# Optimization experiments

Hardware: AMD Instinct MI355X
Metric: run time of the kernel (lower is better)

The kernel has to match this reference:

```python
import jax, jax.numpy as jnp
import numpy as np

N_NODES = 131072
N_EDGES = 1048576
N_FEAT = 8
H = 128
H6 = 256
N_PROB = 64


def _gru_cell(m, h, Wih, Whh, bih, bhh):
    # PyTorch GRUCell semantics
    gi = m @ Wih.T + bih  # [N, 3H]
    gh = h @ Whh.T + bhh
    i_r, i_z, i_n = jnp.split(gi, 3, axis=-1)
    h_r, h_z, h_n = jnp.split(gh, 3, axis=-1)
    r = jax.nn.sigmoid(i_r + h_r)
    z = jax.nn.sigmoid(i_z + h_z)
    n = jnp.tanh(i_n + r * h_n)
    return (1.0 - z) * n + z * h


def _gated_graph_conv(x, src, dst, ew, W, Wih, Whh, bih, bhh):
    # PyG GatedGraphConv(out_channels=H, num_layers=2); in_channels == out_channels so no padding
    h = x
    for l in range(2):
        t = h @ W[l]                      # node-level transform [N, H]
        msg = t[src] * ew[:, None]        # gather + edge scaling [E, H]
        agg = jax.ops.segment_sum(msg, dst, num_segments=x.shape[0])  # scatter-add
        h = _gru_cell(agg, h, Wih, Whh, bih, bhh)
    return h


def _forward(G, edge_index, edge_weight, edge_attribute, segment_ids,
             W_emb1, b_emb1, W_emb2, b_emb2,
             conv1_W, conv1_Wih, conv1_Whh, conv1_bih, conv1_bhh,
             conv2_W, conv2_Wih, conv2_Whh, conv2_bih, conv2_bhh,
             W_g1, b_g1, W_g2, b_g2, W_l, b_l, W_l2, b_l2, W_l3, b_l3):
    src, dst = edge_index[0], edge_index[1]
    x = jax.nn.relu(G @ W_emb1 + b_emb1)
    x = jax.nn.relu(x @ W_emb2 + b_emb2)
    x = jax.nn.relu(_gated_graph_conv(x, src, dst, edge_weight, conv1_W, conv1_Wih, conv1_Whh, conv1_bih, conv1_bhh))
    x = jax.nn.relu(_gated_graph_conv(x, src, dst, edge_weight, conv2_W, conv2_Wih, conv2_Whh, conv2_bih, conv2_bhh))
    x = jax.nn.relu(x @ W_g1 + b_g1)
    x = x @ W_g2 + b_g2                   # node embeddings [N, H]
    # per-problem segment mean (replaces the python loop over contiguous slices)
    sums = jax.ops.segment_sum(x, segment_ids, num_segments=N_PROB)
    counts = jax.ops.segment_sum(jnp.ones((x.shape[0], 1), x.dtype), segment_ids, num_segments=N_PROB)
    gmean = sums / jnp.maximum(counts, 1.0)
    u = jnp.concatenate([x, gmean[segment_ids]], axis=-1)  # [N, 2H]
    u = jax.nn.relu(u @ W_l + b_l)
    u = jax.nn.relu(u @ W_l2 + b_l2)
    u = u @ W_l3 + b_l3                   # [N, 1]
    return u


def setup_inputs() -> dict:
    key = jax.random.key(0)
    ks = jax.random.split(key, 40)
    s = 0.05
    rn = lambda k, shp: (jax.random.normal(k, shp, jnp.float32) * s)
    inp = {}
    inp["G"] = jax.random.normal(ks[0], (N_NODES, N_FEAT), jnp.float32)
    inp["edge_index"] = jax.random.randint(ks[1], (2, N_EDGES), 0, N_NODES, jnp.int32)
    inp["edge_weight"] = jax.random.uniform(ks[2], (N_EDGES,), jnp.float32)
    inp["edge_attribute"] = jax.random.normal(ks[3], (N_EDGES,), jnp.float32)
    inp["segment_ids"] = jnp.sort(jax.random.randint(ks[4], (N_NODES,), 0, N_PROB, jnp.int32))
    inp["W_emb1"] = rn(ks[5], (N_FEAT, H)); inp["b_emb1"] = jnp.zeros((H,), jnp.float32)
    inp["W_emb2"] = rn(ks[6], (H, H));      inp["b_emb2"] = jnp.zeros((H,), jnp.float32)
    inp["conv1_W"] = rn(ks[7], (2, H, H))
    inp["conv1_Wih"] = rn(ks[8], (3 * H, H)); inp["conv1_Whh"] = rn(ks[9], (3 * H, H))
    inp["conv1_bih"] = jnp.zeros((3 * H,), jnp.float32); inp["conv1_bhh"] = jnp.zeros((3 * H,), jnp.float32)
    inp["conv2_W"] = rn(ks[10], (2, H, H))
    inp["conv2_Wih"] = rn(ks[11], (3 * H, H)); inp["conv2_Whh"] = rn(ks[12], (3 * H, H))
    inp["conv2_bih"] = jnp.zeros((3 * H,), jnp.float32); inp["conv2_bhh"] = jnp.zeros((3 * H,), jnp.float32)
    inp["W_g1"] = rn(ks[13], (H, H)); inp["b_g1"] = jnp.zeros((H,), jnp.float32)
    inp["W_g2"] = rn(ks[14], (H, H)); inp["b_g2"] = jnp.zeros((H,), jnp.float32)
    inp["W_l"] = rn(ks[15], (2 * H, H6)); inp["b_l"] = jnp.zeros((H6,), jnp.float32)
    inp["W_l2"] = rn(ks[16], (H6, H)); inp["b_l2"] = jnp.zeros((H,), jnp.float32)
    inp["W_l3"] = rn(ks[17], (H, 1)); inp["b_l3"] = jnp.zeros((1,), jnp.float32)
    return inp


def reference(G, edge_index, edge_weight, edge_attribute, segment_ids,
              W_emb1, b_emb1, W_emb2, b_emb2,
              conv1_W, conv1_Wih, conv1_Whh, conv1_bih, conv1_bhh,
              conv2_W, conv2_Wih, conv2_Whh, conv2_bih, conv2_bhh,
              W_g1, b_g1, W_g2, b_g2, W_l, b_l, W_l2, b_l2, W_l3, b_l3):
    return _forward(G, edge_index, edge_weight, edge_attribute, segment_ids,
                    W_emb1, b_emb1, W_emb2, b_emb2,
                    conv1_W, conv1_Wih, conv1_Whh, conv1_bih, conv1_bhh,
                    conv2_W, conv2_Wih, conv2_Whh, conv2_bih, conv2_bhh,
                    W_g1, b_g1, W_g2, b_g2, W_l, b_l, W_l2, b_l2, W_l3, b_l3)
```

## Files before the change

### kernel.cpp

```cpp
#include <hip/hip_runtime.h>
#include <cstdint>
#include <cstddef>

#define NNODES 131072
#define NEDGES 1048576
#define NPROB  64

typedef _Float16 half8 __attribute__((ext_vector_type(8)));
typedef _Float16 half4v __attribute__((ext_vector_type(4)));
typedef _Float16 half2v __attribute__((ext_vector_type(2)));
typedef float float4v __attribute__((ext_vector_type(4)));

__device__ __forceinline__ float fsigm(float x) {
    return __builtin_amdgcn_rcpf(1.0f + __expf(-x));
}
__device__ __forceinline__ float ftanh(float x) {
    return 1.0f - 2.0f * __builtin_amdgcn_rcpf(__expf(2.0f * x) + 1.0f);
}

__device__ __forceinline__ void async16(void* lds, const void* g) {
    __builtin_amdgcn_global_load_lds(
        (const __attribute__((address_space(1))) uint32_t*)g,
        (__attribute__((address_space(3))) uint32_t*)lds, 16, 0, 0);
}

__global__ __launch_bounds__(256) void tr_cvt2(const float* __restrict__ s0,
    const float* __restrict__ s1, _Float16* __restrict__ dst)
{
    int i = blockIdx.x * 256 + threadIdx.x;
    int half = i >> 14, r = i & 16383;
    int m = r >> 7, k = r & 127;
    const float* s = half ? s1 : s0;
    dst[i] = (_Float16)s[(size_t)k * 128 + m];
}

__global__ __launch_bounds__(256) void tr_cvt(const float* __restrict__ src,
    _Float16* __restrict__ dst, int K, int M, int sstride)
{
    int i = blockIdx.x * 256 + threadIdx.x;
    if (i < M * K) {
        int m = i / K, k = i % K;
        dst[i] = (_Float16)src[(size_t)k * sstride + m];
    }
}

__global__ __launch_bounds__(256) void cvt16_2(const float* __restrict__ a,
    const float* __restrict__ b, _Float16* __restrict__ d)
{
    int i = blockIdx.x * 256 + threadIdx.x;
    d[i] = (_Float16)((i < 49152) ? a[i] : b[i - 49152]);
}

__global__ __launch_bounds__(256) void combine_gru4(const float* __restrict__ W1ih,
    const float* __restrict__ W1, const float* __restrict__ W2ih,
    const float* __restrict__ W2, _Float16* __restrict__ outw)
{
    int i = blockIdx.x * 256 + threadIdx.x;
    int set = i / 49152, r = i - set * 49152;
    int g = r >> 7, j = r & 127;
    const float* Wih = (set < 2) ? W1ih : W2ih;
    const float* W = (set == 0) ? W1 : (set == 1) ? W1 + 16384
                   : (set == 2) ? W2 : W2 + 16384;
    const float* a = Wih + (size_t)g * 128;
    const float* b = W + (size_t)j * 128;
    float s = 0.0f;
#pragma unroll 8
    for (int k = 0; k < 128; ++k) s = fmaf(a[k], b[k], s);
    outw[i] = (_Float16)s;
}

__global__ __launch_bounds__(256) void combine_headA(const float* __restrict__ Wg2,
    const float* __restrict__ Wl, _Float16* __restrict__ At)
{
    int i = blockIdx.x * 256 + threadIdx.x;
    int m = i >> 7, j = i & 127;
    float s = 0.0f;
#pragma unroll 8
    for (int k = 0; k < 128; ++k)
        s = fmaf(Wg2[(size_t)j * 128 + k], Wl[(size_t)k * 256 + m], s);
    At[i] = (_Float16)s;
}

__global__ __launch_bounds__(256) void combine_headB(const float* __restrict__ Wg2,
    const float* __restrict__ Wl, float* __restrict__ Bf)
{
    int i = blockIdx.x * 256 + threadIdx.x;
    int t = i >> 8, m = i & 255;
    float s = 0.0f;
#pragma unroll 8
    for (int k = 0; k < 128; ++k)
        s = fmaf(Wg2[(size_t)t * 128 + k], Wl[(size_t)(128 + k) * 256 + m], s);
    Bf[i] = s;
}

__global__ __launch_bounds__(256) void combine_c(const float* __restrict__ bg2,
    const float* __restrict__ Wl, const float* __restrict__ bl, float* __restrict__ cvec)
{
    int m = threadIdx.x;
    float s = bl[m];
#pragma unroll 8
    for (int k = 0; k < 128; ++k)
        s = fmaf(bg2[k], Wl[(size_t)k * 256 + m] + Wl[(size_t)(128 + k) * 256 + m], s);
    cvec[m] = s;
}

__global__ __launch_bounds__(256) void deg_hist(const int* __restrict__ dst,
                                                int* __restrict__ deg)
{
    int e = blockIdx.x * 256 + threadIdx.x;
    atomicAdd(&deg[dst[e]], 1);
}

__global__ __launch_bounds__(256) void scan1(const int* __restrict__ deg,
    int* __restrict__ offs, int* __restrict__ bsum)
{
    __shared__ int s[256];
    int b = blockIdx.x, tid = threadIdx.x;
    int4 v = ((const int4*)deg)[b * 256 + tid];
    int t0 = v.x, t1 = t0 + v.y, t2 = t1 + v.z, t3 = t2 + v.w;
    s[tid] = t3;
    __syncthreads();
    for (int off = 1; off < 256; off <<= 1) {
        int x = (tid >= off) ? s[tid - off] : 0;
        __syncthreads();
        if (tid >= off) s[tid] += x;
        __syncthreads();
    }
    int excl = tid ? s[tid - 1] : 0;
    int4 o; o.x = excl; o.y = excl + t0; o.z = excl + t1; o.w = excl + t2;
    ((int4*)offs)[b * 256 + tid] = o;
    if (tid == 255) bsum[b] = s[255];
}

__global__ __launch_bounds__(128) void scan2(int* __restrict__ bsum)
{
    __shared__ int s[128];
    int tid = threadIdx.x;
    s[tid] = bsum[tid];
    __syncthreads();
    for (int off = 1; off < 128; off <<= 1) {
        int x = (tid >= off) ? s[tid - off] : 0;
        __syncthreads();
        if (tid >= off) s[tid] += x;
        __syncthreads();
    }
    bsum[tid] = tid ? s[tid - 1] : 0;
}

__global__ __launch_bounds__(256) void scan3(int* __restrict__ offs,
    const int* __restrict__ bsum, int* __restrict__ pos)
{
    int i = blockIdx.x * 256 + threadIdx.x;
    int v = offs[i] + bsum[i >> 10];
    offs[i] = v;
    pos[i] = v;
    if (i == 0) offs[NNODES] = NEDGES;
}

__global__ __launch_bounds__(256) void csr_fill(const int* __restrict__ src,
    const int* __restrict__ dst, const float* __restrict__ ew,
    int* __restrict__ pos, int2* __restrict__ csr)
{
    int e = blockIdx.x * 256 + threadIdx.x;
    int slot = atomicAdd(&pos[dst[e]], 1);
    unsigned long long pk = (unsigned long long)(unsigned)src[e]
                          | ((unsigned long long)__float_as_uint(ew[e]) << 32);
    __builtin_nontemporal_store(pk, (unsigned long long*)csr + slot);
}

__global__ __launch_bounds__(256) void gather_agg(const _Float16* __restrict__ t,
    const int2* __restrict__ csr, const int* __restrict__ offs,
    _Float16* __restrict__ agg)
{
    int node = blockIdx.x * 4 + (threadIdx.x >> 6);
    int lane = threadIdx.x & 63;
    int i = offs[node], end = offs[node + 1];
    float a0 = 0.0f, a1 = 0.0f;
    for (; i + 4 <= end; i += 4) {
        int2 e0 = csr[i], e1 = csr[i + 1], e2 = csr[i + 2], e3 = csr[i + 3];
        half2v v0 = *(const half2v*)(t + (size_t)e0.x * 128 + lane * 2);
        half2v v1 = *(const half2v*)(t + (size_t)e1.x * 128 + lane * 2);
        half2v v2 = *(const half2v*)(t + (size_t)e2.x * 128 + lane * 2);
        half2v v3 = *(const half2v*)(t + (size_t)e3.x * 128 + lane * 2);
        float w0 = __int_as_float(e0.y), w1 = __int_as_float(e1.y);
        float w2 = __int_as_float(e2.y), w3 = __int_as_float(e3.y);
        a0 = fmaf((float)v0[0], w0, a0); a1 = fmaf((float)v0[1], w0, a1);
        a0 = fmaf((float)v1[0], w1, a0); a1 = fmaf((float)v1[1], w1, a1);
        a0 = fmaf((float)v2[0], w2, a0); a1 = fmaf((float)v2[1], w2, a1);
        a0 = fmaf((float)v3[0], w3, a0); a1 = fmaf((float)v3[1], w3, a1);
    }
    for (; i < end; ++i) {
        int2 e = csr[i];
        float w = __int_as_float(e.y);
        half2v v = *(const half2v*)(t + (size_t)e.x * 128 + lane * 2);
        a0 = fmaf((float)v[0], w, a0);
        a1 = fmaf((float)v[1], w, a1);
    }
    half2v o; o[0] = (_Float16)a0; o[1] = (_Float16)a1;
    *(half2v*)(agg + (size_t)node * 128 + lane * 2) = o;
}

__global__ __launch_bounds__(256) void emb1_kernel(const float* __restrict__ G,
    const float* __restrict__ W1, const float* __restrict__ b1, _Float16* __restrict__ Y)
{
    int idx = blockIdx.x * 256 + threadIdx.x;
    int n = idx >> 7, c = idx & 127;
    const float* g = G + (size_t)n * 8;
    float y = b1[c];
#pragma unroll
    for (int k = 0; k < 8; ++k) y = fmaf(g[k], W1[k * 128 + c], y);
    Y[(size_t)n * 128 + c] = (_Float16)fmaxf(y, 0.0f);
}

template<int K, int MCH, bool INF16, bool RELU, bool SEGADD, bool FINAL>
__global__ __launch_bounds__(256, 2) void gemm_mfma(
    const void* __restrict__ Xin, int xstride,
    const _Float16* __restrict__ Wt,
    const float* __restrict__ bias,
    _Float16* __restrict__ out1, int ostride,
    const float* __restrict__ gproj, const int* __restrict__ seg,
    const float* __restrict__ wl3, const float* __restrict__ bl3p,
    float* __restrict__ outf)
{
    constexpr int ROWB = 2 * K;
    constexpr int SPR  = K / 8;
    __shared__ __align__(16) char Xs[128 * ROWB];
    __shared__ __align__(16) char Ws[128 * ROWB];
    const int tid = threadIdx.x, wid = tid >> 6, l = tid & 63;
    const int lr = l & 15, lk = l >> 4;
    const int wrow = wid * 32;

    for (int mc = 0; mc < MCH; ++mc) {
        __syncthreads();
        {
            const _Float16* wsrc = Wt + (size_t)mc * 128 * K;
            for (int s0 = wid * 64; s0 < 128 * SPR; s0 += 256) {
                int s = s0 + l;
                int row = s / SPR, sub = s % SPR;
                int ksub = sub ^ (row & 7);
                async16(Ws + s0 * 16, (const char*)(wsrc + (size_t)row * K) + ksub * 16);
            }
        }
        asm volatile("s_waitcnt vmcnt(0)" ::: "memory");
        __syncthreads();

        half8 bfr[32];
        if constexpr (K == 128) {
#pragma unroll
            for (int ct = 0; ct < 8; ++ct)
#pragma unroll
                for (int ks = 0; ks < 4; ++ks) {
                    int row = ct * 16 + lr;
                    bfr[ct * 4 + ks] = *(const half8*)(Ws + row * ROWB +
                        ((ks * 64 + lk * 16) ^ ((row & 7) << 4)));
                }
        }

        for (int t = blockIdx.x; t < NNODES / 128; t += gridDim.x) {
            const int nbase = t * 128;
            __syncthreads();
            if constexpr (INF16) {
                const _Float16* xsrc = (const _Float16*)Xin;
                for (int s0 = wid * 64; s0 < 128 * SPR; s0 += 256) {
                    int s = s0 + l;
                    int row = s / SPR, sub = s % SPR;
                    int ksub = sub ^ (row & 7);
                    async16(Xs + s0 * 16,
                            (const char*)(xsrc + (size_t)(nbase + row) * xstride) + ksub * 16);
                }
                asm volatile("s_waitcnt vmcnt(0)" ::: "memory");
            } else {
                const float* xsrc = (const float*)Xin;
                for (int s = tid; s < 128 * SPR; s += 256) {
                    int row = s / SPR, sub = s % SPR;
                    int ksub = sub ^ (row & 7);
                    const float* p = xsrc + (size_t)(nbase + row) * xstride + ksub * 8;
                    float4 u = ((const float4*)p)[0];
                    float4 v = ((const float4*)p)[1];
                    half8 hv;
                    hv[0] = (_Float16)u.x; hv[1] = (_Float16)u.y;
                    hv[2] = (_Float16)u.z; hv[3] = (_Float16)u.w;
                    hv[4] = (_Float16)v.x; hv[5] = (_Float16)v.y;
                    hv[6] = (_Float16)v.z; hv[7] = (_Float16)v.w;
                    *(half8*)(Xs + s * 16) = hv;
                }
            }
            __syncthreads();

            float4v acc[2][8];
#pragma unroll
            for (int i = 0; i < 2; ++i)
#pragma unroll
                for (int j = 0; j < 8; ++j)
#pragma unroll
                    for (int q = 0; q < 4; ++q) acc[i][j][q] = 0.0f;

            if constexpr (K == 128) {
#pragma unroll
                for (int rt = 0; rt < 2; ++rt) {
                    half8 a[4];
                    int row = wrow + rt * 16 + lr;
#pragma unroll
                    for (int ks = 0; ks < 4; ++ks)
                        a[ks] = *(const half8*)(Xs + row * ROWB +
                            ((ks * 64 + lk * 16) ^ ((row & 7) << 4)));
#pragma unroll
                    for (int ct = 0; ct < 8; ++ct)
#pragma unroll
                        for (int ks = 0; ks < 4; ++ks)
                            acc[rt][ct] = __builtin_amdgcn_mfma_f32_16x16x32_f16(
                                a[ks], bfr[ct * 4 + ks], acc[rt][ct], 0, 0, 0);
                }
            } else {
#pragma unroll
                for (int kc = 0; kc < 2; ++kc) {
#pragma unroll
                    for (int ct = 0; ct < 8; ++ct)
#pragma unroll
                        for (int ks = 0; ks < 4; ++ks) {
                            int row = ct * 16 + lr;
                            bfr[ct * 4 + ks] = *(const half8*)(Ws + row * ROWB +
                                (((kc * 4 + ks) * 64 + lk * 16) ^ ((row & 7) << 4)));
                        }
#pragma unroll
                    for (int rt = 0; rt < 2; ++rt) {
                        half8 a[4];
                        int row = wrow + rt * 16 + lr;
#pragma unroll
                        for (int ks = 0; ks < 4; ++ks)
                            a[ks] = *(const half8*)(Xs + row * ROWB +
                                (((kc * 4 + ks) * 64 + lk * 16) ^ ((row & 7) << 4)));
#pragma unroll
                        for (int ct = 0; ct < 8; ++ct)
#pragma unroll
                            for (int ks = 0; ks < 4; ++ks)
                                acc[rt][ct] = __builtin_amdgcn_mfma_f32_16x16x32_f16(
                                    a[ks], bfr[ct * 4 + ks], acc[rt][ct], 0, 0, 0);
                    }
                }
            }

            if constexpr (FINAL) {
                const float bl3v = bl3p[0];
                float part[2][4];
#pragma unroll
                for (int rt = 0; rt < 2; ++rt)
#pragma unroll
                    for (int j = 0; j < 4; ++j) part[rt][j] = 0.0f;
#pragma unroll
                for (int rt = 0; rt < 2; ++rt)
#pragma unroll
                for (int ct = 0; ct < 8; ++ct) {
                    const int col = ct * 16 + lr;
                    const float wv = wl3[col];
                    const float bv = bias[col];
#pragma unroll
                    for (int j = 0; j < 4; ++j) {
                        float v = fmaxf(acc[rt][ct][j] + bv, 0.0f);
                        part[rt][j] = fmaf(v, wv, part[rt][j]);
                    }
                }
#pragma unroll
                for (int rt = 0; rt < 2; ++rt)
#pragma unroll
                for (int j = 0; j < 4; ++j) {
                    float s = part[rt][j];
                    s += __shfl_xor(s, 1);
                    s += __shfl_xor(s, 2);
                    s += __shfl_xor(s, 4);
                    s += __shfl_xor(s, 8);
                    if (lr == 0)
                        outf[nbase + wrow + rt * 16 + lk * 4 + j] = s + bl3v;
                }
            } else {
#pragma unroll
                for (int rt = 0; rt < 2; ++rt)
#pragma unroll
                for (int ct = 0; ct < 8; ++ct) {
                    const int col = ct * 16 + lr;
                    float bv = 0.0f;
                    if (bias) bv = bias[mc * 128 + col];
#pragma unroll
                    for (int j = 0; j < 4; ++j) {
                        const int n = nbase + wrow + rt * 16 + lk * 4 + j;
                        float v = acc[rt][ct][j] + bv;
                        if constexpr (SEGADD)
                            v += gproj[(size_t)seg[n] * 256 + mc * 128 + col];
                        if constexpr (RELU) v = fmaxf(v, 0.0f);
                        out1[(size_t)n * ostride + mc * 128 + col] = (_Float16)v;
                    }
                }
            }
        }
    }
}

__global__ __launch_bounds__(512, 2) void gru_fused(
    const _Float16* __restrict__ agg,
    _Float16* h,
    const _Float16* __restrict__ Wc,
    const _Float16* __restrict__ Whh,
    const float* __restrict__ bih, const float* __restrict__ bhh,
    int relu_out)
{
    __shared__ __align__(16) char As[128 * 256];
    __shared__ __align__(16) char Hs[128 * 256];
    __shared__ __align__(16) char Wb[2][128 * 256];
    const int tid = threadIdx.x, wid = tid >> 6, l = tid & 63;
    const int lr = l & 15, lk = l >> 4;
    const int wr = wid >> 1, wc = wid & 1;
    const int nbase = blockIdx.x * 128;

    auto stageT = [&](char* dst, const _Float16* src) {
        for (int s0 = wid * 64; s0 < 2048; s0 += 512) {
            int s = s0 + l;
            int row = s >> 4, sub = s & 15;
            int ksub = sub ^ (row & 7);
            async16(dst + s0 * 16, (const char*)(src + (size_t)row * 128) + ksub * 16);
        }
    };

    stageT(As, agg + (size_t)nbase * 128);
    stageT(Hs, h + (size_t)nbase * 128);
    stageT(Wb[0], Wc);

    float4v accA[2][4], accB[2][4], rg[2][4], zg[2][4];
    half8 aAg[2][4], aH[2][4];

#pragma unroll
    for (int c = 0; c < 6; ++c) {
        asm volatile("s_waitcnt vmcnt(0)" ::: "memory");
        __syncthreads();
        if (c < 5) {
            const int nc = c + 1;
            const _Float16* wsrc = ((nc & 1) ? Whh : Wc) + (size_t)(nc >> 1) * 16384;
            stageT(Wb[nc & 1], wsrc);
        }
        if (c == 0) {
#pragma unroll
            for (int rt = 0; rt < 2; ++rt) {
                const int row = wr * 32 + rt * 16 + lr;
#pragma unroll
                for (int ks = 0; ks < 4; ++ks) {
                    const int off = row * 256 + ((ks * 64 + lk * 16) ^ ((row & 7) << 4));
                    aAg[rt][ks] = *(const half8*)(As + off);
                    aH[rt][ks]  = *(const half8*)(Hs + off);
                }
            }
        }

        auto& af  = (c & 1) ? aH : aAg;
        auto& acc = (c & 1) ? accB : accA;
#pragma unroll
        for (int rt = 0; rt < 2; ++rt)
#pragma unroll
            for (int ct = 0; ct < 4; ++ct)
#pragma unroll
                for (int q = 0; q < 4; ++q) acc[rt][ct][q] = 0.0f;

        const char* wb = Wb[c & 1];
#pragma unroll
        for (int ct = 0; ct < 4; ++ct) {
            const int rowb = wc * 64 + ct * 16 + lr;
#pragma unroll
            for (int ks = 0; ks < 4; ++ks) {
                half8 b = *(const half8*)(wb + rowb * 256 +
                    ((ks * 64 + lk * 16) ^ ((rowb & 7) << 4)));
                acc[0][ct] = __builtin_amdgcn_mfma_f32_16x16x32_f16(af[0][ks], b, acc[0][ct], 0, 0, 0);
                acc[1][ct] = __builtin_amdgcn_mfma_f32_16x16x32_f16(af[1][ks], b, acc[1][ct], 0, 0, 0);
            }
        }

        if (c == 1) {
#pragma unroll
            for (int rt = 0; rt < 2; ++rt)
#pragma unroll
            for (int ct = 0; ct < 4; ++ct) {
                const int col = wc * 64 + ct * 16 + lr;
                const float bb = bih[col] + bhh[col];
#pragma unroll
                for (int j = 0; j < 4; ++j)
                    rg[rt][ct][j] = fsigm(accA[rt][ct][j] + accB[rt][ct][j] + bb);
            }
        } else if (c == 3) {
#pragma unroll
            for (int rt = 0; rt < 2; ++rt)
#pragma unroll
            for (int ct = 0; ct < 4; ++ct) {
                const int col = wc * 64 + ct * 16 + lr;
                const float bb = bih[128 + col] + bhh[128 + col];
#pragma unroll
                for (int j = 0; j < 4; ++j)
                    zg[rt][ct][j] = fsigm(accA[rt][ct][j] + accB[rt][ct][j] + bb);
            }
        } else if (c == 5) {
#pragma unroll
            for (int rt = 0; rt < 2; ++rt)
#pragma unroll
            for (int ct = 0; ct < 4; ++ct) {
                const int col = wc * 64 + ct * 16 + lr;
                const float bi = bih[256 + col], bh = bhh[256 + col];
                const int c2 = col * 2;
#pragma unroll
                for (int j = 0; j < 4; ++j) {
                    const int row = wr * 32 + rt * 16 + lk * 4 + j;
                    const int n = nbase + row;
                    float nv = ftanh(accA[rt][ct][j] + bi +
                                     rg[rt][ct][j] * (accB[rt][ct][j] + bh));
                    float hold = (float)*(const _Float16*)(Hs + row * 256 +
                        (((c2 >> 4) ^ (row & 7)) << 4) + (c2 & 15));
                    float z = zg[rt][ct][j];
                    float hn = (1.0f - z) * nv + z * hold;
                    if (relu_out) hn = fmaxf(hn, 0.0f);
                    h[(size_t)n * 128 + col] = (_Float16)hn;
                }
            }
        }
    }
}

__global__ __launch_bounds__(256) void seg_sum(const _Float16* __restrict__ x,
    const int* __restrict__ seg, float* __restrict__ sums, float* __restrict__ counts)
{
    int cg = threadIdx.x & 31, rs = threadIdx.x >> 5;
    int r0 = blockIdx.x * 256 + rs * 32;
    float a0 = 0, a1 = 0, a2 = 0, a3 = 0, cnt = 0;
    int cur = seg[r0];
    for (int i = 0; i < 32; ++i) {
        int n = r0 + i;
        int p = seg[n];
        if (p != cur) {
            atomicAdd(&sums[(size_t)cur * 128 + cg * 4 + 0], a0);
            atomicAdd(&sums[(size_t)cur * 128 + cg * 4 + 1], a1);
            atomicAdd(&sums[(size_t)cur * 128 + cg * 4 + 2], a2);
            atomicAdd(&sums[(size_t)cur * 128 + cg * 4 + 3], a3);
            if (cg == 0) atomicAdd(&counts[cur], cnt);
            a0 = a1 = a2 = a3 = 0; cnt = 0; cur = p;
        }
        half4v v = *(const half4v*)(x + (size_t)n * 128 + cg * 4);
        a0 += (float)v[0]; a1 += (float)v[1]; a2 += (float)v[2]; a3 += (float)v[3];
        cnt += 1.0f;
    }
    atomicAdd(&sums[(size_t)cur * 128 + cg * 4 + 0], a0);
    atomicAdd(&sums[(size_t)cur * 128 + cg * 4 + 1], a1);
    atomicAdd(&sums[(size_t)cur * 128 + cg * 4 + 2], a2);
    atomicAdd(&sums[(size_t)cur * 128 + cg * 4 + 3], a3);
    if (cg == 0) atomicAdd(&counts[cur], cnt);
}

__global__ __launch_bounds__(256) void gproj2_kernel(const float* __restrict__ sums,
    const float* __restrict__ counts, const float* __restrict__ Bf,
    const float* __restrict__ cvec, float* __restrict__ gproj2)
{
    __shared__ float gm[128];
    int p = blockIdx.x, m = threadIdx.x;
    if (m < 128) gm[m] = sums[(size_t)p * 128 + m] / fmaxf(counts[p], 1.0f);
    __syncthreads();
    float acc = cvec[m];
#pragma unroll 8
    for (int k = 0; k < 128; ++k)
        acc = fmaf(gm[k], Bf[(size_t)k * 256 + m], acc);
    gproj2[(size_t)p * 256 + m] = acc;
}

extern "C" void kernel_launch(void* const* d_in, const int* in_sizes, int n_in,
                              void* d_out, int out_size, void* d_ws, size_t ws_size,
                              hipStream_t stream)
{
    (void)in_sizes; (void)n_in; (void)out_size; (void)ws_size;

    const float* G     = (const float*)d_in[0];
    const int*   ei    = (const int*)d_in[1];
    const float* ew    = (const float*)d_in[2];
    const int*   seg   = (const int*)d_in[4];
    const float* Wemb1 = (const float*)d_in[5];  const float* bemb1 = (const float*)d_in[6];
    const float* Wemb2 = (const float*)d_in[7];  const float* bemb2 = (const float*)d_in[8];
    const float* c1W   = (const float*)d_in[9];
    const float* c1Wih = (const float*)d_in[10]; const float* c1Whh = (const float*)d_in[11];
    const float* c1bih = (const float*)d_in[12]; const float* c1bhh = (const float*)d_in[13];
    const float* c2W   = (const float*)d_in[14];
    const float* c2Wih = (const float*)d_in[15]; const float* c2Whh = (const float*)d_in[16];
    const float* c2bih = (const float*)d_in[17]; const float* c2bhh = (const float*)d_in[18];
    const float* Wg1   = (const float*)d_in[19]; const float* bg1   = (const float*)d_in[20];
    const float* Wg2   = (const float*)d_in[21]; const float* bg2   = (const float*)d_in[22];
    const float* Wl    = (const float*)d_in[23]; const float* bl    = (const float*)d_in[24];
    const float* Wl2   = (const float*)d_in[25]; const float* bl2   = (const float*)d_in[26];
    const float* Wl3   = (const float*)d_in[27]; const float* bl3   = (const float*)d_in[28];

    const int* srcp = ei;
    const int* dstp = ei + NEDGES;

    char* ws = (char*)d_ws;
    const size_t NBH = (size_t)NNODES * 128 * 2;
    const size_t U1B = (size_t)NNODES * 256 * 2;

    _Float16* hA   = (_Float16*)ws;
    _Float16* hB   = (_Float16*)(ws + NBH);
    _Float16* u1   = (_Float16*)(ws + 2 * NBH);
    _Float16* aggH = (_Float16*)(ws + 2 * NBH + U1B);
    char*     aux  = ws + 3 * NBH + U1B;
    float* sums    = (float*)aux;
    float* counts  = (float*)(aux + 32768);
    float* gproj2  = (float*)(aux + 33792);
    int*   deg     = (int*)(aux + 33792 + 65536);
    int*   offs    = deg + NNODES;
    int*   pos     = offs + NNODES + 64;
    int2*  csr     = (int2*)(pos + NNODES);
    char*  wtb     = (char*)csr + (size_t)NEDGES * 8;

    _Float16* wt_emb2 = (_Float16*)wtb;
    _Float16* wt_g1   = wt_emb2 + 16384;
    _Float16* wt_l2   = wt_g1 + 16384;
    _Float16* wt_hh1  = wt_l2 + 32768;
    _Float16* wt_hh2  = wt_hh1 + 49152;
    _Float16* wc0     = wt_hh2 + 49152;
    _Float16* At      = wc0 + 4 * 49152;
    float*    Bf      = (float*)(At + 32768);
    float*    cvec    = Bf + 32768;

    tr_cvt2<<<128, 256, 0, stream>>>(Wemb2, Wg1, wt_emb2);
    tr_cvt<<<128, 256, 0, stream>>>(Wl2, wt_l2, 256, 128, 128);
    cvt16_2<<<384, 256, 0, stream>>>(c1Whh, c2Whh, wt_hh1);
    combine_gru4<<<768, 256, 0, stream>>>(c1Wih, c1W, c2Wih, c2W, wc0);
    combine_headA<<<128, 256, 0, stream>>>(Wg2, Wl, At);
    combine_headB<<<128, 256, 0, stream>>>(Wg2, Wl, Bf);
    combine_c<<<1, 256, 0, stream>>>(bg2, Wl, bl, cvec);

    hipMemsetAsync(deg, 0, NNODES * 4, stream);
    deg_hist<<<NEDGES / 256, 256, 0, stream>>>(dstp, deg);
    scan1<<<128, 256, 0, stream>>>(deg, offs, pos);
    scan2<<<1, 128, 0, stream>>>(pos);
    scan3<<<NNODES / 256, 256, 0, stream>>>(offs, pos, deg);
    csr_fill<<<NEDGES / 256, 256, 0, stream>>>(srcp, dstp, ew, deg, csr);

    emb1_kernel<<<NNODES * 128 / 256, 256, 0, stream>>>(G, Wemb1, bemb1, hB);
    gemm_mfma<128, 1, true, true, false, false><<<512, 256, 0, stream>>>(
        hB, 128, wt_emb2, bemb2, hA, 128, nullptr, nullptr, nullptr, nullptr, nullptr);

    const _Float16* wcs[2][2] = { { wc0, wc0 + 49152 }, { wc0 + 2 * 49152, wc0 + 3 * 49152 } };
    const _Float16* whh[2] = { wt_hh1, wt_hh2 };
    const float* bihs[2] = { c1bih, c2bih };
    const float* bhhs[2] = { c1bhh, c2bhh };
    for (int cv = 0; cv < 2; ++cv) {
        for (int lyr = 0; lyr < 2; ++lyr) {
            gather_agg<<<NNODES / 4, 256, 0, stream>>>(hA, csr, offs, aggH);
            gru_fused<<<NNODES / 128, 512, 0, stream>>>(
                aggH, hA, wcs[cv][lyr], whh[cv], bihs[cv], bhhs[cv], (lyr == 1) ? 1 : 0);
        }
    }

    gemm_mfma<128, 1, true, true, false, false><<<512, 256, 0, stream>>>(
        hA, 128, wt_g1, bg1, hB, 128, nullptr, nullptr, nullptr, nullptr, nullptr);

    hipMemsetAsync(sums, 0, 33792, stream);
    seg_sum<<<NNODES / 256, 256, 0, stream>>>(hB, seg, sums, counts);
    gproj2_kernel<<<NPROB, 256, 0, stream>>>(sums, counts, Bf, cvec, gproj2);

    gemm_mfma<128, 2, true, true, true, false><<<512, 256, 0, stream>>>(
        hB, 128, At, nullptr, u1, 256, gproj2, seg, nullptr, nullptr, nullptr);
    gemm_mfma<256, 1, true, true, false, true><<<256, 256, 0, stream>>>(
        u1, 256, wt_l2, bl2, nullptr, 0, nullptr, nullptr, Wl3, bl3, (float*)d_out);
}
```

Before: 934.9 us.

## Shrink GRU tile to 64 rows with single weight buffer, deepen gather unroll

The fused GRU kernel now handles 64 nodes per block instead of 128 and keeps one weight buffer instead of two. This cuts shared memory per block so more blocks fit per CU (launch bounds raised to 4). The cost is that weight prefetch no longer overlaps with MFMA compute, each weight chunk is re-staged by twice as many blocks, and an extra barrier is added per chunk. Separately, the gather kernel gets an 8-way unrolled loop to keep more independent loads in flight, and the CSR fill drops its nontemporal packed store for a plain int2 store.

```diff
diff --git a/kernel.cpp b/kernel.cpp
--- a/kernel.cpp
+++ b/kernel.cpp
@@ -163,9 +163,7 @@
 {
     int e = blockIdx.x * 256 + threadIdx.x;
     int slot = atomicAdd(&pos[dst[e]], 1);
-    unsigned long long pk = (unsigned long long)(unsigned)src[e]
-                          | ((unsigned long long)__float_as_uint(ew[e]) << 32);
-    __builtin_nontemporal_store(pk, (unsigned long long*)csr + slot);
+    csr[slot] = make_int2(src[e], __float_as_int(ew[e]));
 }
 
 __global__ __launch_bounds__(256) void gather_agg(const _Float16* __restrict__ t,
@@ -176,18 +174,35 @@
     int lane = threadIdx.x & 63;
     int i = offs[node], end = offs[node + 1];
     float a0 = 0.0f, a1 = 0.0f;
+    for (; i + 8 <= end; i += 8) {
+        int2 e[8];
+#pragma unroll
+        for (int k = 0; k < 8; ++k) e[k] = csr[i + k];
+        half2v v[8];
+#pragma unroll
+        for (int k = 0; k < 8; ++k)
+            v[k] = *(const half2v*)(t + (size_t)e[k].x * 128 + lane * 2);
+#pragma unroll
+        for (int k = 0; k < 8; ++k) {
+            float w = __int_as_float(e[k].y);
+            a0 = fmaf((float)v[k][0], w, a0);
+            a1 = fmaf((float)v[k][1], w, a1);
+        }
+    }
     for (; i + 4 <= end; i += 4) {
-        int2 e0 = csr[i], e1 = csr[i + 1], e2 = csr[i + 2], e3 = csr[i + 3];
-        half2v v0 = *(const half2v*)(t + (size_t)e0.x * 128 + lane * 2);
-        half2v v1 = *(const half2v*)(t + (size_t)e1.x * 128 + lane * 2);
-        half2v v2 = *(const half2v*)(t + (size_t)e2.x * 128 + lane * 2);
-        half2v v3 = *(const half2v*)(t + (size_t)e3.x * 128 + lane * 2);
-        float w0 = __int_as_float(e0.y), w1 = __int_as_float(e1.y);
-        float w2 = __int_as_float(e2.y), w3 = __int_as_float(e3.y);
-        a0 = fmaf((float)v0[0], w0, a0); a1 = fmaf((float)v0[1], w0, a1);
-        a0 = fmaf((float)v1[0], w1, a0); a1 = fmaf((float)v1[1], w1, a1);
-        a0 = fmaf((float)v2[0], w2, a0); a1 = fmaf((float)v2[1], w2, a1);
-        a0 = fmaf((float)v3[0], w3, a0); a1 = fmaf((float)v3[1], w3, a1);
+        int2 e[4];
+#pragma unroll
+        for (int k = 0; k < 4; ++k) e[k] = csr[i + k];
+        half2v v[4];
+#pragma unroll
+        for (int k = 0; k < 4; ++k)
+            v[k] = *(const half2v*)(t + (size_t)e[k].x * 128 + lane * 2);
+#pragma unroll
+        for (int k = 0; k < 4; ++k) {
+            float w = __int_as_float(e[k].y);
+            a0 = fmaf((float)v[k][0], w, a0);
+            a1 = fmaf((float)v[k][1], w, a1);
+        }
     }
     for (; i < end; ++i) {
         int2 e = csr[i];
@@ -395,7 +410,7 @@
     }
 }
 
-__global__ __launch_bounds__(512, 2) void gru_fused(
+__global__ __launch_bounds__(512, 4) void gru_fused(
     const _Float16* __restrict__ agg,
     _Float16* h,
     const _Float16* __restrict__ Wc,
@@ -403,39 +418,45 @@
     const float* __restrict__ bih, const float* __restrict__ bhh,
     int relu_out)
 {
-    __shared__ __align__(16) char As[128 * 256];
-    __shared__ __align__(16) char Hs[128 * 256];
-    __shared__ __align__(16) char Wb[2][128 * 256];
+    __shared__ __align__(16) char As[64 * 256];
+    __shared__ __align__(16) char Hs[64 * 256];
+    __shared__ __align__(16) char Wb[128 * 256];
     const int tid = threadIdx.x, wid = tid >> 6, l = tid & 63;
     const int lr = l & 15, lk = l >> 4;
-    const int wr = wid >> 1, wc = wid & 1;
-    const int nbase = blockIdx.x * 128;
-
-    auto stageT = [&](char* dst, const _Float16* src) {
+    const int wr = wid >> 2, wc = wid & 3;
+    const int nbase = blockIdx.x * 64;
+
+    auto stage64 = [&](char* dst, const _Float16* src) {
+        for (int s0 = wid * 64; s0 < 1024; s0 += 512) {
+            int s = s0 + l;
+            int row = s >> 4, sub = s & 15;
+            int ksub = sub ^ (row & 7);
+            async16(dst + s0 * 16, (const char*)(src + (size_t)row * 128) + ksub * 16);
+        }
+    };
+    auto stageW = [&](const _Float16* src) {
         for (int s0 = wid * 64; s0 < 2048; s0 += 512) {
             int s = s0 + l;
             int row = s >> 4, sub = s & 15;
             int ksub = sub ^ (row & 7);
-            async16(dst + s0 * 16, (const char*)(src + (size_t)row * 128) + ksub * 16);
+            async16(Wb + s0 * 16, (const char*)(src + (size_t)row * 128) + ksub * 16);
         }
     };
 
-    stageT(As, agg + (size_t)nbase * 128);
-    stageT(Hs, h + (size_t)nbase * 128);
-    stageT(Wb[0], Wc);
-
-    float4v accA[2][4], accB[2][4], rg[2][4], zg[2][4];
+    float4v accA[2][2], accB[2][2], rg[2][2], zg[2][2];
     half8 aAg[2][4], aH[2][4];
 
 #pragma unroll
     for (int c = 0; c < 6; ++c) {
+        if (c) __syncthreads();
+        stageW(((c & 1) ? Whh : Wc) + (size_t)(c >> 1) * 16384);
+        if (c == 0) {
+            stage64(As, agg + (size_t)nbase * 128);
+            stage64(Hs, h + (size_t)nbase * 128);
+        }
         asm volatile("s_waitcnt vmcnt(0)" ::: "memory");
         __syncthreads();
-        if (c < 5) {
-            const int nc = c + 1;
-            const _Float16* wsrc = ((nc & 1) ? Whh : Wc) + (size_t)(nc >> 1) * 16384;
-            stageT(Wb[nc & 1], wsrc);
-        }
+
         if (c == 0) {
 #pragma unroll
             for (int rt = 0; rt < 2; ++rt) {
@@ -454,17 +475,16 @@
 #pragma unroll
         for (int rt = 0; rt < 2; ++rt)
 #pragma unroll
-            for (int ct = 0; ct < 4; ++ct)
+            for (int ct = 0; ct < 2; ++ct)
 #pragma unroll
                 for (int q = 0; q < 4; ++q) acc[rt][ct][q] = 0.0f;
 
-        const char* wb = Wb[c & 1];
-#pragma unroll
-        for (int ct = 0; ct < 4; ++ct) {
-            const int rowb = wc * 64 + ct * 16 + lr;
+#pragma unroll
+        for (int ct = 0; ct < 2; ++ct) {
+            const int rowb = wc * 32 + ct * 16 + lr;
 #pragma unroll
             for (int ks = 0; ks < 4; ++ks) {
-                half8 b = *(const half8*)(wb + rowb * 256 +
+                half8 b = *(const half8*)(Wb + rowb * 256 +
                     ((ks * 64 + lk * 16) ^ ((rowb & 7) << 4)));
                 acc[0][ct] = __builtin_amdgcn_mfma_f32_16x16x32_f16(af[0][ks], b, acc[0][ct], 0, 0, 0);
                 acc[1][ct] = __builtin_amdgcn_mfma_f32_16x16x32_f16(af[1][ks], b, acc[1][ct], 0, 0, 0);
@@ -475,8 +495,8 @@
 #pragma unroll
             for (int rt = 0; rt < 2; ++rt)
 #pragma unroll
-            for (int ct = 0; ct < 4; ++ct) {
-                const int col = wc * 64 + ct * 16 + lr;
+            for (int ct = 0; ct < 2; ++ct) {
+                const int col = wc * 32 + ct * 16 + lr;
                 const float bb = bih[col] + bhh[col];
 #pragma unroll
                 for (int j = 0; j < 4; ++j)
@@ -486,8 +506,8 @@
 #pragma unroll
             for (int rt = 0; rt < 2; ++rt)
 #pragma unroll
-            for (int ct = 0; ct < 4; ++ct) {
-                const int col = wc * 64 + ct * 16 + lr;
+            for (int ct = 0; ct < 2; ++ct) {
+                const int col = wc * 32 + ct * 16 + lr;
                 const float bb = bih[128 + col] + bhh[128 + col];
 #pragma unroll
                 for (int j = 0; j < 4; ++j)
@@ -497,8 +517,8 @@
 #pragma unroll
             for (int rt = 0; rt < 2; ++rt)
 #pragma unroll
-            for (int ct = 0; ct < 4; ++ct) {
-                const int col = wc * 64 + ct * 16 + lr;
+            for (int ct = 0; ct < 2; ++ct) {
+                const int col = wc * 32 + ct * 16 + lr;
                 const float bi = bih[256 + col], bh = bhh[256 + col];
                 const int c2 = col * 2;
 #pragma unroll
@@ -644,7 +664,7 @@
     for (int cv = 0; cv < 2; ++cv) {
         for (int lyr = 0; lyr < 2; ++lyr) {
             gather_agg<<<NNODES / 4, 256, 0, stream>>>(hA, csr, offs, aggH);
-            gru_fused<<<NNODES / 128, 512, 0, stream>>>(
+            gru_fused<<<NNODES / 64, 512, 0, stream>>>(
                 aggH, hA, wcs[cv][lyr], whh[cv], bihs[cv], bhhs[cv], (lyr == 1) ? 1 : 0);
         }
     }
```

Measured after the change: 1.046 ms. +11.9%, slower.
